# Performance work log

Measured on AMD Instinct MI355X. Metric: run time of the kernel, lower is better.

## Reference

```python
import jax, jax.numpy as jnp
import numpy as np
import math

HEAD_SIZE = 64
WINDOW = 512  # sliding_window_size


def setup_inputs() -> dict:
    key = jax.random.key(0)
    k1, k2, k3, k4 = jax.random.split(key, 4)
    B, T, C = 4, 4096, 1024
    x = jax.random.normal(k1, (B, T, C), dtype=jnp.float32)
    # torch nn.Linear(C, head_size, bias=False) computes x @ W.T with W [hs, C];
    # we store the transposed [C, hs] layout so projection is x @ w.
    s = 1.0 / math.sqrt(C)
    w_key = jax.random.uniform(k2, (C, HEAD_SIZE), jnp.float32, -s, s)
    w_query = jax.random.uniform(k3, (C, HEAD_SIZE), jnp.float32, -s, s)
    w_value = jax.random.uniform(k4, (C, HEAD_SIZE), jnp.float32, -s, s)
    return {"x": x, "w_key": w_key, "w_query": w_query, "w_value": w_value}


def reference(x, w_key, w_query, w_value):
    # Non-cache path (use_cache=False): keys/values are the fresh projections,
    # q_start = k_start = 0, win_size = sliding_window_size.
    B, T, C = x.shape
    q = x @ w_query          # [B, T, hs]
    k = x @ w_key            # [B, T, hs]
    v = x @ w_value          # [B, T, hs]

    # attn_scores = q @ k^T  -> [B, T, T]
    scores = jnp.einsum('btd,bsd->bts', q, k)

    # Sliding-window causal mask: invalid where diff < 0 or diff >= window,
    # with diff = q_pos - k_pos.
    pos = jnp.arange(T)
    diff = pos[:, None] - pos[None, :]          # [T, T]
    mask_bool = (diff < 0) | (diff >= WINDOW)

    scale = math.sqrt(HEAD_SIZE)
    scores = jnp.where(mask_bool[None, :, :], -jnp.inf, scores)
    attn = jax.nn.softmax(scores / scale, axis=-1)  # dropout p=0.0 -> identity

    out = jnp.einsum('bts,bsd->btd', attn, v)   # [B, T, hs]
    return out
```

## Files before the change

kernel.cpp:

```cpp
#include <hip/hip_runtime.h>
#include <hip/hip_bf16.h>
#include <math.h>

#define BB 4
#define TT 4096
#define CC 1024
#define HS 64
#define WIN 512
#define NROW (BB*TT)

typedef float f32x4 __attribute__((ext_vector_type(4)));
typedef short bf16x8 __attribute__((ext_vector_type(8)));

#define MFMA16(a, b, c) __builtin_amdgcn_mfma_f32_16x16x32_bf16((a), (b), (c), 0, 0, 0)

#define GLOAD_LDS(gp, lp) __builtin_amdgcn_global_load_lds( \
    (const __attribute__((address_space(1))) void*)(gp), \
    (__attribute__((address_space(3))) void*)(lp), 16, 0, 0)

__device__ inline unsigned short f2b(float f) {
  union { __hip_bfloat16 h; unsigned short u; } v;
  v.h = __float2bfloat16(f);
  return v.u;
}

__global__ __launch_bounds__(256) void pack_w_kernel(
    const float* __restrict__ wq, const float* __restrict__ wk,
    const float* __restrict__ wv, unsigned short* __restrict__ wp)
{
  int t = blockIdx.x * 256 + threadIdx.x;
  int kg = t / 48;
  int nq = t % 48;
  int n0 = nq * 4;
  int m  = n0 >> 6;
  int c  = n0 & 63;
  const float* w = (m == 0) ? wq : (m == 1) ? wk : wv;
  float4 v = *(const float4*)&w[(size_t)kg * HS + c];
  int kt = kg >> 5;
  int hi = (kg >> 3) & 3;
  int j  = kg & 7;
  float vals[4] = {v.x, v.y, v.z, v.w};
  #pragma unroll
  for (int i = 0; i < 4; ++i) {
    int n  = n0 + i;
    int nb = n >> 4;
    int rl = n & 15;
    int lane = hi * 16 + rl;
    wp[((size_t)(kt * 12 + nb) * 64 + lane) * 8 + j] = f2b(vals[i]);
  }
}

__global__ __launch_bounds__(256) void proj_mfma_kernel(
    const float* __restrict__ x, const unsigned short* __restrict__ wp,
    unsigned short* __restrict__ q_ws, unsigned short* __restrict__ k_ws,
    unsigned short* __restrict__ vt_ws)
{
  __shared__ unsigned char xbuf[3][8192];

  const int tid = threadIdx.x;
  const int l   = tid & 63;
  const int cq  = tid >> 6;
  const int rl  = l & 15;
  const int hi  = l >> 4;
  const int r0  = blockIdx.x * 32;

  f32x4 acc[2][3];
  #pragma unroll
  for (int g = 0; g < 2; ++g)
    #pragma unroll
    for (int j = 0; j < 3; ++j) acc[g][j] = (f32x4){0.f, 0.f, 0.f, 0.f};

#define SX(KS, BUF) { \
    _Pragma("unroll") \
    for (int r = 0; r < 2; ++r) { \
      int s    = r * 256 + tid; \
      int row  = s >> 4; \
      int cpos = s & 15; \
      int cg   = cpos ^ ((row & 7) << 1); \
      GLOAD_LDS(x + (size_t)(r0 + row) * CC + (KS) * 64 + cg * 4, \
                &xbuf[BUF][s * 16]); \
    } }

#define LW(KS, WD) { \
    _Pragma("unroll") \
    for (int ktl = 0; ktl < 2; ++ktl) \
      _Pragma("unroll") \
      for (int j = 0; j < 3; ++j) \
        WD[ktl][j] = *(const bf16x8*)(wp + \
            ((size_t)((KS) * 24 + ktl * 12 + cq * 3 + j) * 64 + l) * 8); }

#define COMP(BUF, WD) { \
    _Pragma("unroll") \
    for (int ktl = 0; ktl < 2; ++ktl) { \
      bf16x8 afr[2]; \
      _Pragma("unroll") \
      for (int g = 0; g < 2; ++g) { \
        int row = g * 16 + rl; \
        int sw  = (row & 7) << 1; \
        int c0  = ktl * 8 + hi * 2; \
        const unsigned char* rb = &xbuf[BUF][row * 256]; \
        f32x4 a0 = *(const f32x4*)(rb + ((c0 ^ sw) * 16)); \
        f32x4 a1 = *(const f32x4*)(rb + (((c0 + 1) ^ sw) * 16)); \
        bf16x8 af; \
        af[0] = (short)f2b(a0[0]); af[1] = (short)f2b(a0[1]); \
        af[2] = (short)f2b(a0[2]); af[3] = (short)f2b(a0[3]); \
        af[4] = (short)f2b(a1[0]); af[5] = (short)f2b(a1[1]); \
        af[6] = (short)f2b(a1[2]); af[7] = (short)f2b(a1[3]); \
        afr[g] = af; \
      } \
      _Pragma("unroll") \
      for (int j = 0; j < 3; ++j) { \
        acc[0][j] = MFMA16(afr[0], WD[ktl][j], acc[0][j]); \
        acc[1][j] = MFMA16(afr[1], WD[ktl][j], acc[1][j]); \
      } \
    } }

#define PHASE_WAIT(N) { \
    asm volatile("s_waitcnt vmcnt(" #N ")" ::: "memory"); \
    __builtin_amdgcn_sched_barrier(0); \
    __builtin_amdgcn_s_barrier(); }

#define PHASE_END { \
    asm volatile("s_waitcnt lgkmcnt(0)" ::: "memory"); \
    __builtin_amdgcn_sched_barrier(0); \
    __builtin_amdgcn_s_barrier(); }

  bf16x8 wA[2][3], wB[2][3];

  SX(0, 0) SX(1, 1) SX(2, 2)
  LW(0, wA) LW(1, wB)

  #pragma unroll 1
  for (int ks = 0; ks < 16; ks += 2) {
    const int bufA = ks % 3;
    const int bufB = (ks + 1) % 3;
    PHASE_WAIT(6)
    COMP(bufA, wA)
    PHASE_END
    if (ks + 3 <= 15) { SX(ks + 3, (ks + 3) % 3) }
    if (ks + 2 <= 15) { LW(ks + 2, wA) }
    __builtin_amdgcn_sched_barrier(0);
    if (ks + 1 < 15) { PHASE_WAIT(6) } else { PHASE_WAIT(0) }
    COMP(bufB, wB)
    PHASE_END
    if (ks + 4 <= 15) { SX(ks + 4, (ks + 4) % 3) }
    if (ks + 3 <= 15) { LW(ks + 3, wB) }
    __builtin_amdgcn_sched_barrier(0);
  }
#undef SX
#undef LW
#undef COMP
#undef PHASE_WAIT
#undef PHASE_END

  #pragma unroll
  for (int g = 0; g < 2; ++g) {
    int rb = r0 + g * 16;
    #pragma unroll
    for (int j = 0; j < 3; ++j) {
      int nb = cq * 3 + j;
      if (nb < 8) {
        unsigned short* dst = (nb < 4) ? q_ws : k_ws;
        int c = (nb & 3) * 16 + rl;
        #pragma unroll
        for (int r = 0; r < 4; ++r) {
          int row = rb + hi * 4 + r;
          dst[(size_t)row * HS + c] = f2b(acc[g][j][r]);
        }
      } else {
        int ch   = rb >> 6;
        int key0 = (rb & 63) + hi * 4;
        int d = (nb - 8) * 16 + rl;
        unsigned u0 = (unsigned)f2b(acc[g][j][0]) | ((unsigned)f2b(acc[g][j][1]) << 16);
        unsigned u1 = (unsigned)f2b(acc[g][j][2]) | ((unsigned)f2b(acc[g][j][3]) << 16);
        uint2 uu; uu.x = u0; uu.y = u1;
        *(uint2*)(vt_ws + (size_t)ch * 4096 + d * 64 + key0) = uu;
      }
    }
  }
}

__global__ __launch_bounds__(256) void attn_mfma_kernel(
    const unsigned short* __restrict__ q_ws, const unsigned short* __restrict__ k_ws,
    const unsigned short* __restrict__ vt_ws, float* __restrict__ out)
{
  __shared__ uint4 smem4[1600];
  unsigned char* smem = (unsigned char*)smem4;

  const int tid = threadIdx.x;
  const int l   = tid & 63;
  const int wid = tid >> 6;
  const int rl  = l & 15;
  const int hi  = l >> 4;
  const int b   = blockIdx.x >> 6;
  const int qt  = blockIdx.x & 63;
  const int t0  = qt * 64;
  const int t0w = t0 + wid * 16;

  const unsigned short* qrow = q_ws + (size_t)(b * TT + t0w + rl) * HS;
  bf16x8 qb0 = *(const bf16x8*)(qrow + hi * 8);
  bf16x8 qb1 = *(const bf16x8*)(qrow + 32 + hi * 8);

  f32x4 oacc[4];
  #pragma unroll
  for (int i = 0; i < 4; ++i) oacc[i] = (f32x4){0.f, 0.f, 0.f, 0.f};
  float m_run = -INFINITY, l_run = 0.f;

  int s_lo = t0 - WIN; if (s_lo < 0) s_lo = 0;
  unsigned char* pbase = smem + 16384 + wid * 2304 + rl * 144;

  for (int sc = s_lo; sc < t0 + 64; sc += 64) {
    __syncthreads();
    {
      const unsigned short* kg = k_ws + (size_t)(b * TT + sc) * HS;
      const unsigned short* vg = vt_ws + (size_t)((b * TT + sc) >> 6) * 4096;
      #pragma unroll
      for (int i = 0; i < 2; ++i) {
        int idx = tid + i * 256;
        int row = idx >> 3;
        int c16 = idx & 7;
        uint4 kv = *(const uint4*)(kg + row * 64 + c16 * 8);
        uint4 vv = *(const uint4*)(vg + row * 64 + c16 * 8);
        *(uint4*)(smem + row * 128 + ((c16 ^ (row & 7)) * 16)) = kv;
        *(uint4*)(smem + 8192 + row * 128 + ((c16 ^ (row & 7)) * 16)) = vv;
      }
    }
    __syncthreads();

    f32x4 sacc[4];
    #pragma unroll
    for (int i = 0; i < 4; ++i) sacc[i] = (f32x4){0.f, 0.f, 0.f, 0.f};
    #pragma unroll
    for (int kb = 0; kb < 4; ++kb) {
      int row = kb * 16 + rl;
      unsigned char* kr = smem + row * 128;
      bf16x8 k0 = *(const bf16x8*)(kr + (((hi) ^ (row & 7)) * 16));
      bf16x8 k1 = *(const bf16x8*)(kr + (((4 + hi) ^ (row & 7)) * 16));
      sacc[kb] = MFMA16(k0, qb0, sacc[kb]);
      sacc[kb] = MFMA16(k1, qb1, sacc[kb]);
    }

    const int tg = t0w + rl;
    float p[16];
    float tm = -INFINITY;
    bool full = (sc + 63 <= t0w) && (sc >= t0w - 496);
    #pragma unroll
    for (int kb = 0; kb < 4; ++kb)
      #pragma unroll
      for (int r = 0; r < 4; ++r) {
        float v = sacc[kb][r] * 0.125f;
        if (!full) {
          int key = sc + kb * 16 + hi * 4 + r;
          int diff = tg - key;
          v = (diff >= 0 && diff < WIN) ? v : -INFINITY;
        }
        p[kb * 4 + r] = v;
        tm = fmaxf(tm, v);
      }
    tm = fmaxf(tm, __shfl_xor(tm, 16));
    tm = fmaxf(tm, __shfl_xor(tm, 32));
    float m_new = fmaxf(m_run, tm);
    float fac  = (m_new == -INFINITY) ? 1.f : __expf(m_run - m_new);
    float msub = (m_new == -INFINITY) ? 0.f : m_new;
    float lsum = 0.f;
    #pragma unroll
    for (int i = 0; i < 16; ++i) { p[i] = __expf(p[i] - msub); lsum += p[i]; }
    lsum += __shfl_xor(lsum, 16);
    lsum += __shfl_xor(lsum, 32);
    l_run = l_run * fac + lsum;
    m_run = m_new;

    #pragma unroll
    for (int kb = 0; kb < 4; ++kb) {
      unsigned u0 = (unsigned)f2b(p[kb * 4 + 0]) | ((unsigned)f2b(p[kb * 4 + 1]) << 16);
      unsigned u1 = (unsigned)f2b(p[kb * 4 + 2]) | ((unsigned)f2b(p[kb * 4 + 3]) << 16);
      uint2 uu; uu.x = u0; uu.y = u1;
      *(uint2*)(pbase + kb * 32 + hi * 8) = uu;
    }

    #pragma unroll
    for (int r = 0; r < 4; ++r) {
      float fr = __shfl(fac, (l & 48) | (hi * 4 + r));
      oacc[0][r] *= fr; oacc[1][r] *= fr; oacc[2][r] *= fr; oacc[3][r] *= fr;
    }

    bf16x8 pa0 = *(const bf16x8*)(pbase + hi * 16);
    bf16x8 pa1 = *(const bf16x8*)(pbase + 64 + hi * 16);
    #pragma unroll
    for (int f = 0; f < 4; ++f) {
      int d = f * 16 + rl;
      unsigned char* vr = smem + 8192 + d * 128;
      bf16x8 v0 = *(const bf16x8*)(vr + (((hi) ^ (d & 7)) * 16));
      bf16x8 v1 = *(const bf16x8*)(vr + (((4 + hi) ^ (d & 7)) * 16));
      oacc[f] = MFMA16(pa0, v0, oacc[f]);
      oacc[f] = MFMA16(pa1, v1, oacc[f]);
    }
  }

  float inv = 1.f / l_run;
  #pragma unroll
  for (int r = 0; r < 4; ++r) {
    float ir = __shfl(inv, (l & 48) | (hi * 4 + r));
    int row = b * TT + t0w + hi * 4 + r;
    #pragma unroll
    for (int f = 0; f < 4; ++f)
      out[(size_t)row * HS + f * 16 + rl] = oacc[f][r] * ir;
  }
}

extern "C" void kernel_launch(void* const* d_in, const int* in_sizes, int n_in,
                              void* d_out, int out_size, void* d_ws, size_t ws_size,
                              hipStream_t stream) {
  const float* x  = (const float*)d_in[0];
  const float* wk = (const float*)d_in[1];
  const float* wq = (const float*)d_in[2];
  const float* wv = (const float*)d_in[3];
  float* out = (float*)d_out;

  unsigned short* wp    = (unsigned short*)d_ws;
  unsigned short* q_ws  = wp + 196608;
  unsigned short* k_ws  = q_ws + (size_t)NROW * HS;
  unsigned short* vt_ws = k_ws + (size_t)NROW * HS;

  pack_w_kernel<<<192, 256, 0, stream>>>(wq, wk, wv, wp);
  proj_mfma_kernel<<<NROW / 32, 256, 0, stream>>>(x, wp, q_ws, k_ws, vt_ws);
  attn_mfma_kernel<<<BB * (TT / 64), 256, 0, stream>>>(q_ws, k_ws, vt_ws, out);
}
```

Baseline: 45.56 us.

## Stage projection weights in LDS and double rows per block in projection

The projection kernel now runs 512 threads over 64 rows per block. Packed weights are loaded once per k-step into registers and written to a double-buffered LDS area, so two row-halves share them instead of each wave reading weights from global memory. The x staging ring grows to four buffers and the explicit vmcnt waits before compute are removed. LDS use rises to about 112KB, which allows roughly one block per CU, and relying on compiler-inserted waits for the async LDS loads may leave a cross-thread race.

Result: slower. 49.29 us (+8.2%).

```diff
diff --git a/kernel.cpp b/kernel.cpp
--- a/kernel.cpp
+++ b/kernel.cpp
@@ -50,19 +50,22 @@
   }
 }
 
-__global__ __launch_bounds__(256) void proj_mfma_kernel(
+__global__ __launch_bounds__(512) void proj_mfma_kernel(
     const float* __restrict__ x, const unsigned short* __restrict__ wp,
     unsigned short* __restrict__ q_ws, unsigned short* __restrict__ k_ws,
     unsigned short* __restrict__ vt_ws)
 {
-  __shared__ unsigned char xbuf[3][8192];
+  __shared__ unsigned char xbuf[4][16384];
+  __shared__ unsigned char wbuf[2][24576];
 
   const int tid = threadIdx.x;
   const int l   = tid & 63;
-  const int cq  = tid >> 6;
+  const int wid = tid >> 6;
+  const int cq  = wid & 3;
+  const int rh  = wid >> 2;
   const int rl  = l & 15;
   const int hi  = l >> 4;
-  const int r0  = blockIdx.x * 32;
+  const int r0  = blockIdx.x * 64;
 
   f32x4 acc[2][3];
   #pragma unroll
@@ -73,7 +76,7 @@
 #define SX(KS, BUF) { \
     _Pragma("unroll") \
     for (int r = 0; r < 2; ++r) { \
-      int s    = r * 256 + tid; \
+      int s    = r * 512 + tid; \
       int row  = s >> 4; \
       int cpos = s & 15; \
       int cg   = cpos ^ ((row & 7) << 1); \
@@ -81,24 +84,26 @@
                 &xbuf[BUF][s * 16]); \
     } }
 
-#define LW(KS, WD) { \
+#define LWR(KS, WR) { \
     _Pragma("unroll") \
-    for (int ktl = 0; ktl < 2; ++ktl) \
-      _Pragma("unroll") \
-      for (int j = 0; j < 3; ++j) \
-        WD[ktl][j] = *(const bf16x8*)(wp + \
-            ((size_t)((KS) * 24 + ktl * 12 + cq * 3 + j) * 64 + l) * 8); }
-
-#define COMP(BUF, WD) { \
+    for (int i = 0; i < 3; ++i) \
+      WR[i] = *(const bf16x8*)(wp + (size_t)(KS) * 12288 + (i * 512 + tid) * 8); }
+
+#define WST(WR, BUF) { \
+    _Pragma("unroll") \
+    for (int i = 0; i < 3; ++i) \
+      *(bf16x8*)&wbuf[BUF][(i * 512 + tid) * 16] = WR[i]; }
+
+#define COMP(XB, WB) { \
     _Pragma("unroll") \
     for (int ktl = 0; ktl < 2; ++ktl) { \
       bf16x8 afr[2]; \
       _Pragma("unroll") \
       for (int g = 0; g < 2; ++g) { \
-        int row = g * 16 + rl; \
+        int row = rh * 32 + g * 16 + rl; \
         int sw  = (row & 7) << 1; \
         int c0  = ktl * 8 + hi * 2; \
-        const unsigned char* rb = &xbuf[BUF][row * 256]; \
+        const unsigned char* rb = &xbuf[XB][row * 256]; \
         f32x4 a0 = *(const f32x4*)(rb + ((c0 ^ sw) * 16)); \
         f32x4 a1 = *(const f32x4*)(rb + (((c0 + 1) ^ sw) * 16)); \
         bf16x8 af; \
@@ -110,52 +115,47 @@
       } \
       _Pragma("unroll") \
       for (int j = 0; j < 3; ++j) { \
-        acc[0][j] = MFMA16(afr[0], WD[ktl][j], acc[0][j]); \
-        acc[1][j] = MFMA16(afr[1], WD[ktl][j], acc[1][j]); \
+        bf16x8 wf = *(const bf16x8*)&wbuf[WB][((ktl * 12 + cq * 3 + j) * 64 + l) * 16]; \
+        acc[0][j] = MFMA16(afr[0], wf, acc[0][j]); \
+        acc[1][j] = MFMA16(afr[1], wf, acc[1][j]); \
       } \
     } }
-
-#define PHASE_WAIT(N) { \
-    asm volatile("s_waitcnt vmcnt(" #N ")" ::: "memory"); \
-    __builtin_amdgcn_sched_barrier(0); \
-    __builtin_amdgcn_s_barrier(); }
 
 #define PHASE_END { \
     asm volatile("s_waitcnt lgkmcnt(0)" ::: "memory"); \
     __builtin_amdgcn_sched_barrier(0); \
     __builtin_amdgcn_s_barrier(); }
 
-  bf16x8 wA[2][3], wB[2][3];
+  bf16x8 wrA[3], wrB[3];
 
   SX(0, 0) SX(1, 1) SX(2, 2)
-  LW(0, wA) LW(1, wB)
+  LWR(0, wrA)
+  WST(wrA, 0)
+  LWR(1, wrB)
+  PHASE_END
 
   #pragma unroll 1
   for (int ks = 0; ks < 16; ks += 2) {
-    const int bufA = ks % 3;
-    const int bufB = (ks + 1) % 3;
-    PHASE_WAIT(6)
-    COMP(bufA, wA)
+    if (ks + 3 <= 15) { SX(ks + 3, (ks + 3) & 3) }
+    if (ks + 2 <= 15) { LWR(ks + 2, wrA) }
+    if (ks + 1 <= 15) { WST(wrB, (ks + 1) & 1) }
+    COMP(ks & 3, ks & 1)
     PHASE_END
-    if (ks + 3 <= 15) { SX(ks + 3, (ks + 3) % 3) }
-    if (ks + 2 <= 15) { LW(ks + 2, wA) }
-    __builtin_amdgcn_sched_barrier(0);
-    if (ks + 1 < 15) { PHASE_WAIT(6) } else { PHASE_WAIT(0) }
-    COMP(bufB, wB)
+    if (ks + 4 <= 15) { SX(ks + 4, (ks + 4) & 3) }
+    if (ks + 3 <= 15) { LWR(ks + 3, wrB) }
+    if (ks + 2 <= 15) { WST(wrA, (ks + 2) & 1) }
+    COMP((ks + 1) & 3, (ks + 1) & 1)
     PHASE_END
-    if (ks + 4 <= 15) { SX(ks + 4, (ks + 4) % 3) }
-    if (ks + 3 <= 15) { LW(ks + 3, wB) }
-    __builtin_amdgcn_sched_barrier(0);
   }
 #undef SX
-#undef LW
+#undef LWR
+#undef WST
 #undef COMP
-#undef PHASE_WAIT
 #undef PHASE_END
 
   #pragma unroll
   for (int g = 0; g < 2; ++g) {
-    int rb = r0 + g * 16;
+    int rb = r0 + rh * 32 + g * 16;
     #pragma unroll
     for (int j = 0; j < 3; ++j) {
       int nb = cq * 3 + j;
@@ -323,6 +323,6 @@
   unsigned short* vt_ws = k_ws + (size_t)NROW * HS;
 
   pack_w_kernel<<<192, 256, 0, stream>>>(wq, wk, wv, wp);
-  proj_mfma_kernel<<<NROW / 32, 256, 0, stream>>>(x, wp, q_ws, k_ws, vt_ws);
+  proj_mfma_kernel<<<NROW / 64, 512, 0, stream>>>(x, wp, q_ws, k_ws, vt_ws);
   attn_mfma_kernel<<<BB * (TT / 64), 256, 0, stream>>>(q_ws, k_ws, vt_ws, out);
 }
```
